# Performance work log

Hardware: AMD Instinct MI355X
Metric: run time of the kernel (lower is better)

Reference implementation:

```python
import jax, jax.numpy as jnp
import numpy as np

IMC = 256
EPS = 1e-6
BN_EPS = 1e-5
GRID = (69.12, 79.36)      # (depth, width) in meters
OFF = (0.0, -39.68, 0.0)   # (xoff, yoff, zoff)
RES = 0.64
ZMIN, ZMAX = -3.0, 2.76
SCALES = [0.25, 0.125, 0.0625, 0.03125, 0.015625]


def make_corners():
    # replicates make_grid(): corner lattice in lidar coords, shape [nz, nx, ny, 3]
    nx = int(round(GRID[0] / RES)) + 1   # 109
    ny = int(round(GRID[1] / RES)) + 1   # 125
    nz = int(round((ZMAX - ZMIN) / RES)) + 1  # 10
    xc = RES * np.arange(nx) + OFF[0]
    yc = GRID[1] - RES * np.arange(ny) + OFF[1]
    zc = ZMAX - RES * np.arange(nz)
    xx, yy = np.meshgrid(xc, yc, indexing='ij')
    base = np.stack([xx, yy, np.full_like(xx, OFF[2])], axis=-1)  # [nx,ny,3]
    zoffs = np.stack([np.zeros(nz), np.zeros(nz), zc], axis=-1)   # [nz,3]
    corners = base[None] + zoffs[:, None, None, :]
    return jnp.asarray(corners, jnp.float32)


def grid_sample(img, grid):
    # img [B,C,H,W]; grid [B,P,N,2] xy in [-1,1]; bilinear, zero padding, align_corners=False
    B, C, H, W = img.shape
    x = (grid[..., 0] + 1.0) * (W * 0.5) - 0.5
    y = (grid[..., 1] + 1.0) * (H * 0.5) - 0.5
    x0f = jnp.floor(x); y0f = jnp.floor(y)
    wx = (x - x0f).reshape(B, 1, -1)
    wy = (y - y0f).reshape(B, 1, -1)
    x0 = x0f.astype(jnp.int32); y0 = y0f.astype(jnp.int32)
    flat = img.reshape(B, C, H * W)
    def g(xi, yi):
        ok = ((xi >= 0) & (xi < W) & (yi >= 0) & (yi < H)).reshape(B, 1, -1)
        idx = (jnp.clip(yi, 0, H - 1) * W + jnp.clip(xi, 0, W - 1)).reshape(B, 1, -1)
        return jnp.take_along_axis(flat, idx, axis=2) * ok
    v00 = g(x0, y0); v01 = g(x0 + 1, y0); v10 = g(x0, y0 + 1); v11 = g(x0 + 1, y0 + 1)
    out = (v00 * (1 - wx) + v01 * wx) * (1 - wy) + (v10 * (1 - wx) + v11 * wx) * wy
    return out.reshape(B, C, grid.shape[1], grid.shape[2])


def oft(feats, calib, corners, scale, w, b):
    B, C, Hf, Wf = feats.shape
    # perspective projection of grid corners into the image plane
    hom = jnp.einsum('bij,zdwj->bzdwi', calib[:, :, :3], corners) + calib[:, None, None, None, :, 3]
    xy = hom[..., :2] / hom[..., 2:3]                      # [B,nz,nx,ny,2]
    img_size = jnp.array([Wf, Hf], jnp.float32) / scale
    nc = jnp.clip(2.0 * xy / img_size - 1.0, -1.0, 1.0)
    mn = jnp.minimum(nc[:, :-1, :-1, :-1], nc[:, :-1, 1:, :-1])
    mx = jnp.maximum(nc[:, 1:, 1:, 1:], nc[:, 1:, :-1, 1:])
    bbox = jnp.concatenate([mn, mx], axis=-1)              # [B,Zc,Dc,Wc,4]
    _, Zc, Dc, Wc, _ = bbox.shape
    bbox = bbox.reshape(B, Zc, Dc * Wc, 4)
    area = ((bbox[..., 2] - bbox[..., 0]) * (bbox[..., 3] - bbox[..., 1])
            * (Hf * Wf * 0.25) + EPS)[:, None]             # [B,1,Zc,N]
    visible = (area > EPS).astype(feats.dtype)
    ii = jnp.cumsum(jnp.cumsum(feats, axis=-1), axis=-2)   # integral image
    tl = grid_sample(ii, jnp.stack([bbox[..., 0], bbox[..., 1]], -1))
    br = grid_sample(ii, jnp.stack([bbox[..., 2], bbox[..., 3]], -1))
    tr = grid_sample(ii, jnp.stack([bbox[..., 2], bbox[..., 1]], -1))
    bl = grid_sample(ii, jnp.stack([bbox[..., 0], bbox[..., 3]], -1))
    vox = (tl + br - tr - bl) / area * visible             # [B,C,Zc,N]
    vox = vox.transpose(0, 3, 1, 2).reshape(B * Dc * Wc, C * Zc)
    ortho = jax.nn.relu(vox @ w.T + b).reshape(B, Dc, Wc, -1)
    return ortho.transpose(0, 3, 2, 1)                     # [B,imc,Wc,Dc]


def attention(x, aw, ab):
    s = jax.nn.sigmoid(x.mean(axis=(2, 3)) @ aw.T + ab)
    return x * s[:, :, None, None]


def conv3x3(x, w, stride):
    return jax.lax.conv_general_dilated(x, w, (stride, stride), ((1, 1), (1, 1)),
                                        dimension_numbers=('NCHW', 'OIHW', 'NCHW'))


def bn(x, g, b, m, v):
    scale = g / jnp.sqrt(v + BN_EPS)
    return (x - m[None, :, None, None]) * scale[None, :, None, None] + b[None, :, None, None]


def make_calib(B):
    K = np.array([[560.0, 0.0, 640.0], [0.0, 560.0, 192.0], [0.0, 0.0, 1.0]])
    Rt = np.array([[0.0, -1.0, 0.0, 0.05],   # lidar(x fwd, y left, z up) -> cam(x right, y down, z fwd)
                   [0.0, 0.0, -1.0, -0.30],
                   [1.0, 0.0, 0.0, 0.27]])
    P = K @ Rt
    return jnp.asarray(np.tile(P[None], (B, 1, 1)), jnp.float32)


def setup_inputs() -> dict:
    key = jax.random.key(0)
    ks = jax.random.split(key, 16)
    B = 1
    shapes = [(B, IMC, 96, 320), (B, IMC, 48, 160), (B, IMC, 24, 80), (B, IMC, 12, 40), (B, IMC, 6, 20)]
    feats = [jax.random.normal(ks[i], s, jnp.float32) * 0.1 for i, s in enumerate(shapes)]
    HC = 9 * IMC  # height_channels = int((2.76-(-3))/0.64 * 256) = 2304
    inp = {
        'feats04': feats[0], 'feats08': feats[1], 'feats16': feats[2],
        'feats32': feats[3], 'feats64': feats[4],
        'calib': make_calib(B),
        'oft_w': jax.random.normal(ks[5], (5, IMC, HC), jnp.float32) * 0.02,
        'oft_b': jax.random.normal(ks[6], (5, IMC), jnp.float32) * 0.02,
        'att_w': jax.random.normal(ks[7], (IMC, IMC), jnp.float32) * 0.05,
        'att_b': jnp.zeros((IMC,), jnp.float32),
        'conv1_w': jax.random.normal(ks[8], (IMC, IMC * 5, 3, 3), jnp.float32) * 0.02,
        'bn1_g': 1.0 + 0.1 * jax.random.normal(ks[9], (IMC,), jnp.float32),
        'bn1_b': 0.05 * jax.random.normal(ks[10], (IMC,), jnp.float32),
        'bn1_m': 0.05 * jax.random.normal(ks[11], (IMC,), jnp.float32),
        'bn1_v': jax.random.uniform(ks[12], (IMC,), jnp.float32, 0.5, 1.5),
        'conv2_w': jax.random.normal(ks[13], (IMC, IMC, 3, 3), jnp.float32) * 0.02,
        'bn2_g': 1.0 + 0.1 * jax.random.normal(ks[14], (IMC,), jnp.float32),
        'bn2_b': jnp.zeros((IMC,), jnp.float32),
        'bn2_m': jnp.zeros((IMC,), jnp.float32),
        'bn2_v': jax.random.uniform(ks[15], (IMC,), jnp.float32, 0.5, 1.5),
    }
    return inp


def reference(feats04, feats08, feats16, feats32, feats64, calib,
              oft_w, oft_b, att_w, att_b,
              conv1_w, bn1_g, bn1_b, bn1_m, bn1_v,
              conv2_w, bn2_g, bn2_b, bn2_m, bn2_v):
    corners = make_corners()
    feats = [feats04, feats08, feats16, feats32, feats64]
    orthos = [attention(oft(f, calib, corners, s, oft_w[i], oft_b[i]), att_w, att_b)
              for i, (f, s) in enumerate(zip(feats, SCALES))]
    x = jnp.concatenate(orthos, axis=1)            # [B, 5*imc, 124, 108]
    x = jax.nn.relu(bn(conv3x3(x, conv1_w, 2), bn1_g, bn1_b, bn1_m, bn1_v))
    x = jax.nn.relu(bn(conv3x3(x, conv2_w, 1), bn2_g, bn2_b, bn2_m, bn2_v))
    return x                                       # [B, imc, 62, 54]
```

## Files before the change

kernel.cpp:

```cpp
#include <hip/hip_runtime.h>

typedef __attribute__((ext_vector_type(8))) short short8;
typedef __attribute__((ext_vector_type(4))) float float4v;
typedef __attribute__((ext_vector_type(4))) int int4v;
typedef __attribute__((ext_vector_type(4))) unsigned short ushort4v;

#define NBOX 13392
#define ZC 9
#define KOFT 2304
#define NPIX 3348
#define NBLK0 105
#define NBLKC 27
#define TILEK 4096
#define NBSTRIDE 294912
#define VOXSZ 30965760

__device__ __forceinline__ unsigned short f2bf(float f) {
  union { float f; unsigned int i; } v; v.f = f;
  unsigned int r = v.i + 0x7FFFu + ((v.i >> 16) & 1u);
  return (unsigned short)(r >> 16);
}
__device__ __forceinline__ float bf2f(unsigned short u) {
  union { unsigned int i; float f; } v; v.i = ((unsigned int)u) << 16; return v.f;
}
__device__ __forceinline__ float i2f(int i) {
  union { int i; float f; } v; v.i = i; return v.f;
}

__device__ __forceinline__ const int* uniform_ptr(const int* p) {
  unsigned lo = (unsigned)(uintptr_t)p;
  unsigned hi = (unsigned)((uintptr_t)p >> 32);
  lo = (unsigned)__builtin_amdgcn_readfirstlane((int)lo);
  hi = (unsigned)__builtin_amdgcn_readfirstlane((int)hi);
  return (const int*)(((uintptr_t)hi << 32) | (uintptr_t)lo);
}

__device__ __forceinline__ void async16(const unsigned short* g, unsigned short* l) {
  __builtin_amdgcn_global_load_lds(
      (const __attribute__((address_space(1))) unsigned int*)g,
      (__attribute__((address_space(3))) unsigned int*)l, 16, 0, 0);
}

__global__ void k_alpha_beta(const float* __restrict__ oft_b,
                             const float* __restrict__ g1, const float* __restrict__ b1,
                             const float* __restrict__ m1, const float* __restrict__ v1,
                             const float* __restrict__ g2, const float* __restrict__ b2,
                             const float* __restrict__ m2, const float* __restrict__ v2,
                             float* __restrict__ ALPHA, float* __restrict__ BETA,
                             float* __restrict__ MEANS, unsigned short* __restrict__ ZPAGE) {
  int g = blockIdx.x, c = threadIdx.x;
  float al, be;
  if (g < 5) { al = 1.f; be = oft_b[g * 256 + c]; MEANS[g * 256 + c] = 0.f; }
  else {
    const float* gg = (g == 5) ? g1 : g2;
    const float* bb = (g == 5) ? b1 : b2;
    const float* mm = (g == 5) ? m1 : m2;
    const float* vv = (g == 5) ? v1 : v2;
    al = gg[c] / sqrtf(vv[c] + 1e-5f);
    be = bb[c] - mm[c] * al;
  }
  ALPHA[g * 256 + c] = al; BETA[g * 256 + c] = be;
  if (g == 0) ZPAGE[c] = 0;
}

__global__ void k_wpermT(const float* __restrict__ w, unsigned short* __restrict__ wp) {
  int idx = blockIdx.x * 256 + threadIdx.x;
  int sc = idx / 589824;
  int r  = idx % 589824;
  int j   = r & 7;
  int row = (r >> 3) & 127;
  int kc  = (r >> 10) & 3;
  int cs  = r >> 12;
  int cb  = cs / 72, s = cs % 72;
  int oc = cb * 128 + row;
  int k  = s * 32 + kc * 8 + j;
  int z = k >> 8, c = k & 255;
  wp[idx] = f2bf(w[((size_t)sc * 256 + oc) * 2304 + c * 9 + z]);
}

__global__ void k_wperm1T(const float* __restrict__ w, const float* __restrict__ satt,
                          unsigned short* __restrict__ wp) {
  int idx = blockIdx.x * 256 + threadIdx.x;
  int j   = idx & 7;
  int row = (idx >> 3) & 127;
  int kc  = (idx >> 10) & 3;
  int rest = idx >> 12;
  int s = rest % 40; rest /= 40;
  int r = rest % 9;  int cb = rest / 9;
  int oc = cb * 128 + row;
  int ic = s * 32 + kc * 8 + j;
  wp[idx] = f2bf(w[(size_t)oc * 11520 + ic * 9 + r] * satt[ic]);
}

__global__ void k_wperm2T(const float* __restrict__ w, unsigned short* __restrict__ wp) {
  int idx = blockIdx.x * 256 + threadIdx.x;
  int j   = idx & 7;
  int row = (idx >> 3) & 127;
  int kc  = (idx >> 10) & 3;
  int rest = idx >> 12;
  int s = rest % 8; rest /= 8;
  int r = rest % 9; int cb = rest / 9;
  int oc = cb * 128 + row;
  int ic = s * 32 + kc * 8 + j;
  wp[idx] = f2bf(w[(size_t)oc * 2304 + ic * 9 + r]);
}

__global__ void k_taps(const float* __restrict__ calib, int* __restrict__ taps,
                       int Hf, int Wf, float areaScale) {
  int idx = blockIdx.x * 256 + threadIdx.x;
  if (idx >= ZC * NBOX) return;
  int z = idx / NBOX, n = idx % NBOX;
  int d = n / 124, wj = n % 124;
  float P[12];
#pragma unroll
  for (int i = 0; i < 12; ++i) P[i] = calib[i];
  auto proj = [&](int k, int i, int j, float& nxo, float& nyo) {
    float X = 0.64f * (float)i;
    float Y = 39.68f - 0.64f * (float)j;
    float Z = 2.76f - 0.64f * (float)k;
    float hx = P[0] * X + P[1] * Y + P[2]  * Z + P[3];
    float hy = P[4] * X + P[5] * Y + P[6]  * Z + P[7];
    float hz = P[8] * X + P[9] * Y + P[10] * Z + P[11];
    float px = hx / hz, py = hy / hz;
    nxo = 2.f * px / 1280.f - 1.f; nxo = fminf(fmaxf(nxo, -1.f), 1.f);
    nyo = 2.f * py / 384.f  - 1.f; nyo = fminf(fmaxf(nyo, -1.f), 1.f);
  };
  float ax, ay, bx, by, cx, cy, dx, dy;
  proj(z,     d,     wj,     ax, ay);
  proj(z,     d + 1, wj,     bx, by);
  proj(z + 1, d + 1, wj + 1, cx, cy);
  proj(z + 1, d,     wj + 1, dx, dy);
  float x0 = fminf(ax, bx), y0 = fminf(ay, by);
  float x1 = fmaxf(cx, dx), y1 = fmaxf(cy, dy);
  float rawA = (x1 - x0) * (y1 - y0) * areaScale;
  int* ob = taps + (size_t)idx * 32;
  if (!(rawA > 0.f)) { ob[0] = 0; return; }
  float inv = 1.f / (rawA + 1e-6f);

  float u0 = (x0 + 1.f) * ((float)Wf * 0.5f) - 0.5f;
  float u1 = (x1 + 1.f) * ((float)Wf * 0.5f) - 0.5f;
  float fu0 = floorf(u0), fu1 = floorf(u1);
  int cx0 = (int)fu0, cx1 = (int)fu1;
  float wx0 = u0 - fu0, wx1 = u1 - fu1;
  int xs[4]; float xw[4];
  xs[0] = cx0; xs[1] = cx0 + 1; xs[2] = cx1; xs[3] = cx1 + 1;
  xw[0] = (1.f - wx0) * inv; xw[1] = wx0 * inv;
  xw[2] = -(1.f - wx1) * inv; xw[3] = -wx1 * inv;
  int dcx = cx1 - cx0;
  if (dcx == 0)      { xw[0] += xw[2]; xw[1] += xw[3]; xw[2] = 0.f; xw[3] = 0.f; }
  else if (dcx == 1) { xw[1] += xw[2]; xw[2] = xw[3]; xs[2] = xs[3]; xw[3] = 0.f; }
#pragma unroll
  for (int j = 0; j < 4; ++j) {
    if (xs[j] < 0 || xs[j] >= Wf) xw[j] = 0.f;
    xs[j] = min(max(xs[j], 0), Wf - 1);
  }
#define CSWX(a, b) { if (xw[a] == 0.f && xw[b] != 0.f) { \
    float tw = xw[a]; xw[a] = xw[b]; xw[b] = tw; \
    int ts = xs[a]; xs[a] = xs[b]; xs[b] = ts; } }
  CSWX(0, 1) CSWX(2, 3) CSWX(0, 2) CSWX(1, 3) CSWX(1, 2)
#undef CSWX
  int nx = (xw[0] != 0.f) + (xw[1] != 0.f) + (xw[2] != 0.f) + (xw[3] != 0.f);

  float v0 = (y0 + 1.f) * ((float)Hf * 0.5f) - 0.5f;
  float v1 = (y1 + 1.f) * ((float)Hf * 0.5f) - 0.5f;
  float fv0 = floorf(v0), fv1 = floorf(v1);
  int ry0 = (int)fv0, ry1 = (int)fv1;
  float wy0 = v0 - fv0, wy1 = v1 - fv1;
  int ys[4]; float yw[4];
  ys[0] = ry0; ys[1] = ry0 + 1; ys[2] = ry1; ys[3] = ry1 + 1;
  yw[0] = 1.f - wy0; yw[1] = wy0; yw[2] = -(1.f - wy1); yw[3] = -wy1;
  int dcy = ry1 - ry0;
  if (dcy == 0)      { yw[0] += yw[2]; yw[1] += yw[3]; yw[2] = 0.f; yw[3] = 0.f; }
  else if (dcy == 1) { yw[1] += yw[2]; yw[2] = yw[3]; ys[2] = ys[3]; yw[3] = 0.f; }
#pragma unroll
  for (int j = 0; j < 4; ++j) {
    if (ys[j] < 0 || ys[j] >= Hf) yw[j] = 0.f;
    ys[j] = min(max(ys[j], 0), Hf - 1);
  }
#define CSWY(a, b) { if (yw[a] == 0.f && yw[b] != 0.f) { \
    float tw = yw[a]; yw[a] = yw[b]; yw[b] = tw; \
    int ts = ys[a]; ys[a] = ys[b]; ys[b] = ts; } }
  CSWY(0, 1) CSWY(2, 3) CSWY(0, 2) CSWY(1, 3) CSWY(1, 2)
#undef CSWY
  int ny = (yw[0] != 0.f) + (yw[1] != 0.f) + (yw[2] != 0.f) + (yw[3] != 0.f);

  if (nx == 0 || ny == 0) { ob[0] = 0; return; }

  int off[16]; float w[16];
#pragma unroll
  for (int r = 0; r < 4; ++r)
#pragma unroll
    for (int c = 0; c < 4; ++c) {
      off[r * 4 + c] = (ys[r] * Wf + xs[c]) * 1024;
      w[r * 4 + c] = yw[r] * xw[c];
    }
  off[0] |= (nx << 25) | (ny << 28);
  int4v* obv = (int4v*)ob;
#pragma unroll
  for (int i = 0; i < 4; ++i)
    obv[i] = (int4v){off[4 * i], off[4 * i + 1], off[4 * i + 2], off[4 * i + 3]};
  float4v* wb = (float4v*)obv;
#pragma unroll
  for (int i = 0; i < 4; ++i)
    wb[4 + i] = (float4v){w[4 * i], w[4 * i + 1], w[4 * i + 2], w[4 * i + 3]};
}

__global__ void k_transpose_all(const float* __restrict__ f0, const float* __restrict__ f1,
                                const float* __restrict__ f2, const float* __restrict__ f3,
                                const float* __restrict__ f4, float* __restrict__ II) {
  int b = blockIdx.x;
  int sc, cx;
  if (b < 480)      { sc = 0; cx = b; }
  else if (b < 600) { sc = 1; cx = b - 480; }
  else if (b < 630) { sc = 2; cx = b - 600; }
  else if (b < 638) { sc = 3; cx = b - 630; }
  else              { sc = 4; cx = b - 638; }
  const int Ss[5] = {30720, 7680, 1920, 480, 120};
  const size_t IIof[5] = {0, 7864320, 9830400, 10321920, 10444800};
  const float* srcs[5] = {f0, f1, f2, f3, f4};
  int S = Ss[sc];
  const float* src = srcs[sc];
  float* dst = II + IIof[sc];
  __shared__ float tile[64][65];
  int t = threadIdx.x;
  int wave = t >> 6, lane = t & 63;
  int s0 = cx * 64, c0 = blockIdx.y * 64;
#pragma unroll
  for (int i = 0; i < 16; ++i) {
    int c_l = wave * 16 + i;
    if (s0 + lane < S) tile[c_l][lane] = src[(size_t)(c0 + c_l) * S + s0 + lane];
  }
  __syncthreads();
#pragma unroll
  for (int i = 0; i < 16; ++i) {
    int s_l = wave * 16 + i;
    if (s0 + s_l < S) dst[(size_t)(s0 + s_l) * 256 + c0 + lane] = tile[lane][s_l];
  }
}

__global__ void k_cumw_all(float* __restrict__ II) {
  int b = blockIdx.x;
  int sc, h;
  if (b < 96)       { sc = 0; h = b; }
  else if (b < 144) { sc = 1; h = b - 96; }
  else if (b < 168) { sc = 2; h = b - 144; }
  else if (b < 180) { sc = 3; h = b - 168; }
  else              { sc = 4; h = b - 180; }
  const int Wfs[5] = {320, 160, 80, 40, 20};
  const size_t IIof[5] = {0, 7864320, 9830400, 10321920, 10444800};
  int Wf = Wfs[sc];
  float* p = II + IIof[sc] + (size_t)h * Wf * 256 + threadIdx.x;
  float acc = 0.f;
#pragma unroll 4
  for (int w = 0; w < Wf; ++w) { acc += p[(size_t)w * 256]; p[(size_t)w * 256] = acc; }
}

__global__ void k_cumh_all(float* __restrict__ II) {
  int b = blockIdx.x;
  int sc, w;
  if (b < 320)      { sc = 0; w = b; }
  else if (b < 480) { sc = 1; w = b - 320; }
  else if (b < 560) { sc = 2; w = b - 480; }
  else if (b < 600) { sc = 3; w = b - 560; }
  else              { sc = 4; w = b - 600; }
  const int Wfs[5] = {320, 160, 80, 40, 20};
  const int Hfs[5] = {96, 48, 24, 12, 6};
  const size_t IIof[5] = {0, 7864320, 9830400, 10321920, 10444800};
  int Hf = Hfs[sc];
  size_t stride = (size_t)Wfs[sc] * 256;
  float* p = II + IIof[sc] + (size_t)w * 256 + threadIdx.x;
  float acc = 0.f;
#pragma unroll 4
  for (int h = 0; h < Hf; ++h) { acc += p[h * stride]; p[h * stride] = acc; }
}

__global__ __launch_bounds__(512) void k_sample(const float* __restrict__ ii,
                                                const int* __restrict__ taps,
                                                unsigned short* __restrict__ voxT) {
  __shared__ unsigned short st[3][8][66][4];
  int t = threadIdx.x;
  int wave = t >> 6, lane = t & 63;
  int n = blockIdx.x * 8 + wave;
  int zg = blockIdx.y * 3;
  const char* iib = (const char*)ii + (lane << 4);
#pragma unroll
  for (int dz = 0; dz < 3; ++dz) {
    int z = zg + dz;
    const int* tb = uniform_ptr(taps + (size_t)(z * NBOX + n) * 32);
    int o_[16];
#pragma unroll
    for (int i = 0; i < 16; ++i) o_[i] = tb[i];
    unsigned h = (unsigned)o_[0];
    int nx = (h >> 25) & 7;
    int ny = (h >> 28) & 7;
    o_[0] = (int)(h & 0x01FFFFFFu);
    ushort4v o;
    if (ny == 0) {
      o[0] = 0; o[1] = 0; o[2] = 0; o[3] = 0;
    } else {
      float w_[16];
#pragma unroll
      for (int i = 0; i < 16; ++i) w_[i] = i2f(tb[16 + i]);
      float4v a0 = {0.f, 0.f, 0.f, 0.f}, a1 = a0;
#define TAP(i, acc) { float4v t_ = *(const float4v*)(iib + (size_t)(unsigned)o_[i]); acc += t_ * w_[i]; }
      TAP(0, a0)
      if (nx > 1) TAP(1, a1)
      if (nx > 2) TAP(2, a0)
      if (nx > 3) TAP(3, a1)
      if (ny > 1) {
        TAP(4, a0)
        if (nx > 1) TAP(5, a1)
        if (nx > 2) TAP(6, a0)
        if (nx > 3) TAP(7, a1)
      }
      if (ny > 2) {
        TAP(8, a0)
        if (nx > 1) TAP(9, a1)
        if (nx > 2) TAP(10, a0)
        if (nx > 3) TAP(11, a1)
      }
      if (ny > 3) {
        TAP(12, a0)
        if (nx > 1) TAP(13, a1)
        if (nx > 2) TAP(14, a0)
        if (nx > 3) TAP(15, a1)
      }
#undef TAP
      float4v acc = a0 + a1;
#pragma unroll
      for (int j = 0; j < 4; ++j) o[j] = f2bf(acc[j]);
    }
    *(ushort4v*)&st[dz][wave][lane][0] = o;
  }
  __syncthreads();
  int nb = (blockIdx.x * 8) >> 7;
  int r0 = (blockIdx.x * 8) & 127;
  unsigned short* outb = voxT + (size_t)nb * NBSTRIDE + (size_t)r0 * 32;
  int lane32 = t & 31;
  int row = lane32 >> 2, kc = lane32 & 3;
#pragma unroll
  for (int p = 0; p < 2; ++p) {
    int q = p * 16 + (t >> 5);
    if (q < 24) {
      int zq = q >> 3;
      int si = q & 7;
      short8 v = *(const short8*)&st[zq][row][si * 8 + kc * 2][0];
      *(short8*)(outb + (size_t)(zg + zq) * 32768 + (size_t)si * 4096
                 + (size_t)(row * 32 + kc * 8)) = v;
    }
  }
}

__global__ __launch_bounds__(256) void k_gemmT_all(
    const unsigned short* __restrict__ AT, const unsigned short* __restrict__ BT,
    const float* __restrict__ beta, unsigned short* __restrict__ xbuf, int s0) {
  __shared__ unsigned short ls[8704];
  unsigned short* lsA = ls;
  unsigned short* lsB = ls + 4096;
  int t = threadIdx.x;
  int lane = t & 63, wave = t >> 6;
  int l15 = lane & 15, quad = lane >> 4;
  int nb = blockIdx.x, cb = blockIdx.y;
  int slab = blockIdx.z, sc = s0 + slab;
  int wrow = (wave >> 1) * 64, wcol = (wave & 1) * 64;

  const unsigned short* ga = AT + (size_t)slab * VOXSZ + (size_t)nb * NBSTRIDE + t * 8;
  const unsigned short* gb = BT + (size_t)sc * 589824 + (size_t)cb * NBSTRIDE + t * 8;
  unsigned short* ldA = lsA + t * 8;
  unsigned short* ldB = lsB + t * 8;

  float4v acc[4][4];
#pragma unroll
  for (int mi = 0; mi < 4; ++mi)
#pragma unroll
    for (int ni = 0; ni < 4; ++ni) acc[mi][ni] = (float4v){0.f, 0.f, 0.f, 0.f};

  for (int s = 0; s < 72; ++s) {
    async16(ga, ldA);
    async16(ga + 2048, ldA + 2048);
    async16(gb, ldB);
    async16(gb + 2048, ldB + 2048);
    ga += TILEK; gb += TILEK;
    __syncthreads();
    short8 af[4], bf[4];
    const short8* pA = (const short8*)lsA;
    const short8* pB = (const short8*)lsB;
#pragma unroll
    for (int mi = 0; mi < 4; ++mi) af[mi] = pA[(wrow + mi * 16 + l15) * 4 + quad];
#pragma unroll
    for (int ni = 0; ni < 4; ++ni) bf[ni] = pB[quad * 128 + wcol + ni * 16 + l15];
#pragma unroll
    for (int mi = 0; mi < 4; ++mi)
#pragma unroll
      for (int ni = 0; ni < 4; ++ni)
        acc[mi][ni] = __builtin_amdgcn_mfma_f32_16x16x32_bf16(af[mi], bf[ni], acc[mi][ni], 0, 0, 0);
    __syncthreads();
  }

  float bval[4];
#pragma unroll
  for (int ni = 0; ni < 4; ++ni)
    bval[ni] = beta[sc * 256 + cb * 128 + wcol + ni * 16 + l15];
#pragma unroll
  for (int ph = 0; ph < 2; ++ph) {
    if (wrow == ph * 64) {
#pragma unroll
      for (int mi = 0; mi < 4; ++mi)
#pragma unroll
        for (int ni = 0; ni < 4; ++ni)
#pragma unroll
          for (int j = 0; j < 4; ++j) {
            int row = mi * 16 + quad * 4 + j;
            int col = wcol + ni * 16 + l15;
            float v = acc[mi][ni][j] + bval[ni];
            ls[row * 136 + col] = f2bf(v > 0.f ? v : 0.f);
          }
    }
    __syncthreads();
#pragma unroll
    for (int it = 0; it < 4; ++it) {
      int idx = it * 256 + t;
      int row = idx >> 4, ch = idx & 15;
      int nn = nb * 128 + ph * 64 + row;
      if (nn < NBOX) {
        short8 v = *(const short8*)&ls[row * 136 + ch * 8];
        *(short8*)(xbuf + (size_t)nn * 1280 + sc * 256 + cb * 128 + ch * 8) = v;
      }
    }
    __syncthreads();
  }
}

__global__ __launch_bounds__(256) void k_gemmT(
    const unsigned short* __restrict__ AT, const unsigned short* __restrict__ BT,
    float* __restrict__ part) {
  __shared__ unsigned short lsA[4096];
  __shared__ unsigned short lsB[4096];
  int t = threadIdx.x;
  int lane = t & 63, wave = t >> 6;
  int l15 = lane & 15, quad = lane >> 4;
  int nb = blockIdx.x, cb = blockIdx.y, ks = blockIdx.z;
  int wrow = (wave >> 1) * 64, wcol = (wave & 1) * 64;

  const unsigned short* ga = AT + (size_t)nb * NBSTRIDE + (size_t)ks * 18 * TILEK + t * 8;
  const unsigned short* gb = BT + (size_t)cb * NBSTRIDE + (size_t)ks * 18 * TILEK + t * 8;
  unsigned short* ldA = lsA + t * 8;
  unsigned short* ldB = lsB + t * 8;

  float4v acc[4][4];
#pragma unroll
  for (int mi = 0; mi < 4; ++mi)
#pragma unroll
    for (int ni = 0; ni < 4; ++ni) acc[mi][ni] = (float4v){0.f, 0.f, 0.f, 0.f};

  for (int s = 0; s < 18; ++s) {
    async16(ga, ldA);
    async16(ga + 2048, ldA + 2048);
    async16(gb, ldB);
    async16(gb + 2048, ldB + 2048);
    ga += TILEK; gb += TILEK;
    __syncthreads();
    short8 af[4], bf[4];
    const short8* pA = (const short8*)lsA;
    const short8* pB = (const short8*)lsB;
#pragma unroll
    for (int mi = 0; mi < 4; ++mi) af[mi] = pA[(wrow + mi * 16 + l15) * 4 + quad];
#pragma unroll
    for (int ni = 0; ni < 4; ++ni) bf[ni] = pB[quad * 128 + wcol + ni * 16 + l15];
#pragma unroll
    for (int mi = 0; mi < 4; ++mi)
#pragma unroll
      for (int ni = 0; ni < 4; ++ni)
        acc[mi][ni] = __builtin_amdgcn_mfma_f32_16x16x32_bf16(af[mi], bf[ni], acc[mi][ni], 0, 0, 0);
    __syncthreads();
  }

#pragma unroll
  for (int mi = 0; mi < 4; ++mi) {
    int nb0 = nb * 128 + wrow + mi * 16 + quad * 4;
#pragma unroll
    for (int j = 0; j < 4; ++j) {
      int nn = nb0 + j;
      if (nn < NBOX) {
#pragma unroll
        for (int ni = 0; ni < 4; ++ni) {
          int oc = cb * 128 + wcol + ni * 16 + l15;
          part[((size_t)ks * NBOX + nn) * 256 + oc] = acc[mi][ni][j];
        }
      }
    }
  }
}

__global__ void k_redoft(const float* __restrict__ part, const float* __restrict__ beta,
                         unsigned short* __restrict__ xbuf, int choff) {
  int n = blockIdx.x, oc = threadIdx.x;
  float v = part[(size_t)n * 256 + oc]
          + part[((size_t)NBOX + n) * 256 + oc]
          + part[((size_t)2 * NBOX + n) * 256 + oc]
          + part[((size_t)3 * NBOX + n) * 256 + oc];
  v += beta[oc];
  v = v > 0.f ? v : 0.f;
  xbuf[(size_t)n * 1280 + choff + oc] = f2bf(v);
}

template <int MODE>
__global__ __launch_bounds__(256) void k_gemmS(
    const unsigned short* __restrict__ A, const unsigned short* __restrict__ BT,
    float* __restrict__ part, const unsigned short* __restrict__ zpage) {
  constexpr int KIC   = (MODE == 1) ? 1280 : 256;
  constexpr int STEPS = KIC / 32;
  __shared__ unsigned short lsA[4096];
  __shared__ unsigned short lsB[4096];
  int t = threadIdx.x;
  int lane = t & 63, wave = t >> 6;
  int l15 = lane & 15, quad = lane >> 4;
  int n0 = blockIdx.x * 128, oc0 = blockIdx.y * 128;
  int r = blockIdx.z;
  int wrow = (wave >> 1) * 64, wcol = (wave & 1) * 64;
  int srow = t & 127, skc = t >> 7;

  int p = n0 + srow;
  int oy = p / 54, ox = p - oy * 54;
  int ky = r / 3, kx = r - ky * 3;
  bool valid; int sp;
  if (MODE == 1) {
    int ih = 2 * oy + ky - 1, iw = 2 * ox + kx - 1;
    valid = (p < NPIX) && ((unsigned)ih < 124u) && ((unsigned)iw < 108u);
    sp = iw * 124 + ih;
  } else {
    int ih = oy + ky - 1, iw = ox + kx - 1;
    valid = (p < NPIX) && ((unsigned)ih < 62u) && ((unsigned)iw < 54u);
    sp = ih * 54 + iw;
  }
  const unsigned short* ga = valid ? (A + (size_t)sp * KIC + skc * 8) : zpage;
  int astep = valid ? 32 : 0;
  const unsigned short* gb = BT + ((size_t)(blockIdx.y * 9 + r) * STEPS) * TILEK + t * 8;
  unsigned short* ldA = lsA + t * 8;
  unsigned short* ldB = lsB + t * 8;

  float4v acc[4][4];
#pragma unroll
  for (int mi = 0; mi < 4; ++mi)
#pragma unroll
    for (int ni = 0; ni < 4; ++ni) acc[mi][ni] = (float4v){0.f, 0.f, 0.f, 0.f};

  for (int s = 0; s < STEPS; ++s) {
    async16(ga, ldA);
    async16(ga + 16, ldA + 2048);
    async16(gb, ldB);
    async16(gb + 2048, ldB + 2048);
    ga += astep; gb += TILEK;
    __syncthreads();
    short8 af[4], bf[4];
    const short8* pA = (const short8*)lsA;
    const short8* pB = (const short8*)lsB;
#pragma unroll
    for (int mi = 0; mi < 4; ++mi) af[mi] = pA[quad * 128 + wrow + mi * 16 + l15];
#pragma unroll
    for (int ni = 0; ni < 4; ++ni) bf[ni] = pB[quad * 128 + wcol + ni * 16 + l15];
#pragma unroll
    for (int mi = 0; mi < 4; ++mi)
#pragma unroll
      for (int ni = 0; ni < 4; ++ni)
        acc[mi][ni] = __builtin_amdgcn_mfma_f32_16x16x32_bf16(af[mi], bf[ni], acc[mi][ni], 0, 0, 0);
    __syncthreads();
  }

#pragma unroll
  for (int mi = 0; mi < 4; ++mi) {
    int nb0 = n0 + wrow + mi * 16 + quad * 4;
#pragma unroll
    for (int j = 0; j < 4; ++j) {
      int nn = nb0 + j;
      if (nn < NPIX) {
#pragma unroll
        for (int ni = 0; ni < 4; ++ni) {
          int oc = oc0 + wcol + ni * 16 + l15;
          part[((size_t)r * NPIX + nn) * 256 + oc] = acc[mi][ni][j];
        }
      }
    }
  }
}

template <bool F32OUT>
__global__ void k_redconv(const float* __restrict__ part, const float* __restrict__ alpha,
                          const float* __restrict__ beta, void* __restrict__ outv) {
  int p = blockIdx.x, oc = threadIdx.x;
  float v = 0.f;
#pragma unroll
  for (int r = 0; r < 9; ++r) v += part[((size_t)r * NPIX + p) * 256 + oc];
  v = v * alpha[oc] + beta[oc];
  v = v > 0.f ? v : 0.f;
  if (F32OUT) ((float*)outv)[(size_t)oc * NPIX + p] = v;
  else ((unsigned short*)outv)[(size_t)p * 256 + oc] = f2bf(v);
}

__global__ void k_means2(const unsigned short* __restrict__ x, float* __restrict__ means) {
  int tid = threadIdx.x;
  int r0 = blockIdx.x * 64;
  float part[5] = {0.f, 0.f, 0.f, 0.f, 0.f};
  for (int i = 0; i < 64; ++i) {
    int row = r0 + i;
    if (row < NBOX) {
      const unsigned short* rp = x + (size_t)row * 1280;
#pragma unroll
      for (int g = 0; g < 5; ++g) part[g] += bf2f(rp[g * 256 + tid]);
    }
  }
#pragma unroll
  for (int g = 0; g < 5; ++g) atomicAdd(&means[g * 256 + tid], part[g]);
}

__global__ void k_att(const float* __restrict__ means, const float* __restrict__ aw,
                      const float* __restrict__ ab, float* __restrict__ satt) {
  int sc = blockIdx.x, c = threadIdx.x;
  __shared__ float m[256];
  m[c] = means[sc * 256 + c] * (1.f / (float)NBOX);
  __syncthreads();
  float acc = ab[c];
  for (int j = 0; j < 256; ++j) acc += m[j] * aw[c * 256 + j];
  satt[sc * 256 + c] = 1.f / (1.f + expf(-acc));
}

extern "C" void kernel_launch(void* const* d_in, const int* in_sizes, int n_in,
                              void* d_out, int out_size, void* d_ws, size_t ws_size,
                              hipStream_t stream) {
  const float* feats[5];
  for (int i = 0; i < 5; ++i) feats[i] = (const float*)d_in[i];
  const float* calib   = (const float*)d_in[5];
  const float* oft_w   = (const float*)d_in[6];
  const float* oft_b   = (const float*)d_in[7];
  const float* att_w   = (const float*)d_in[8];
  const float* att_b   = (const float*)d_in[9];
  const float* conv1_w = (const float*)d_in[10];
  const float* bn1g = (const float*)d_in[11];
  const float* bn1b = (const float*)d_in[12];
  const float* bn1m = (const float*)d_in[13];
  const float* bn1v = (const float*)d_in[14];
  const float* conv2_w = (const float*)d_in[15];
  const float* bn2g = (const float*)d_in[16];
  const float* bn2b = (const float*)d_in[17];
  const float* bn2m = (const float*)d_in[18];
  const float* bn2v = (const float*)d_in[19];

  char* ws = (char*)d_ws;
  size_t off = 0;
  auto alloc = [&](size_t bytes) -> void* {
    void* p = ws + off; off += (bytes + 255) & ~(size_t)255; return p;
  };
  unsigned short* WPERMT = (unsigned short*)alloc((size_t)5 * 589824 * 2);
  unsigned short* WC1T   = (unsigned short*)alloc((size_t)2949120 * 2);
  unsigned short* WC2T   = (unsigned short*)alloc((size_t)589824 * 2);
  float*          II     = (float*)alloc((size_t)10475520 * 4);
  unsigned short* XBUF   = (unsigned short*)alloc((size_t)NBOX * 1280 * 2);
  unsigned short* Y1     = (unsigned short*)alloc((size_t)NPIX * 256 * 2);
  float*          MEANS  = (float*)alloc(1280 * 4);
  float*          SATT   = (float*)alloc(1280 * 4);
  float*          ALPHA  = (float*)alloc(7 * 256 * 4);
  float*          BETA   = (float*)alloc(7 * 256 * 4);
  unsigned short* ZPAGE  = (unsigned short*)alloc(256 * 2);

  const size_t SLAB   = (size_t)VOXSZ * 2;
  const size_t TAPSZ  = (size_t)ZC * NBOX * 128;
  const size_t PARTSZ = (size_t)4 * NBOX * 256 * 4;
  size_t rem = (ws_size > off) ? ws_size - off : 0;

  int NS;
  int* TAPS; unsigned short* VOXT; float* PART;
  if (rem >= 5 * SLAB) {
    NS = 5;
    VOXT = (unsigned short*)alloc(5 * SLAB);
    TAPS = (int*)XBUF;
    PART = (float*)VOXT;
  } else if (rem >= 2 * SLAB + TAPSZ) {
    NS = (int)((rem - TAPSZ) / SLAB); if (NS > 4) NS = 4;
    TAPS = (int*)alloc(TAPSZ);
    VOXT = (unsigned short*)alloc((size_t)NS * SLAB);
    PART = (float*)VOXT;
  } else {
    NS = 0;
    VOXT = (unsigned short*)alloc(SLAB);
    PART = (float*)alloc(PARTSZ);
    TAPS = (int*)PART;
  }
  (void)in_sizes; (void)n_in; (void)out_size;

  static const int HFs[5] = {96, 48, 24, 12, 6};
  static const int WFs[5] = {320, 160, 80, 40, 20};
  static const size_t IIoff[5] = {0, 7864320, 9830400, 10321920, 10444800};

  k_alpha_beta<<<7, 256, 0, stream>>>(oft_b, bn1g, bn1b, bn1m, bn1v,
                                      bn2g, bn2b, bn2m, bn2v, ALPHA, BETA, MEANS, ZPAGE);
  k_wpermT<<<11520, 256, 0, stream>>>(oft_w, WPERMT);
  k_wperm2T<<<2304, 256, 0, stream>>>(conv2_w, WC2T);

  k_transpose_all<<<dim3(640, 4), 256, 0, stream>>>(feats[0], feats[1], feats[2],
                                                    feats[3], feats[4], II);
  k_cumw_all<<<186, 256, 0, stream>>>(II);
  k_cumh_all<<<620, 256, 0, stream>>>(II);

  if (NS > 0) {
    int g0 = 0;
    while (g0 < 5) {
      int gsz = 5 - g0; if (gsz > NS) gsz = NS;
      for (int s = g0; s < g0 + gsz; ++s) {
        k_taps<<<(ZC * NBOX + 255) / 256, 256, 0, stream>>>(
            calib, TAPS, HFs[s], WFs[s], (float)(HFs[s] * WFs[s]) * 0.25f);
        k_sample<<<dim3(NBOX / 8, 3), 512, 0, stream>>>(
            II + IIoff[s], TAPS, VOXT + (size_t)(s - g0) * VOXSZ);
      }
      k_gemmT_all<<<dim3(NBLK0, 2, gsz), 256, 0, stream>>>(VOXT, WPERMT, BETA, XBUF, g0);
      g0 += gsz;
    }
  } else {
    for (int s = 0; s < 5; ++s) {
      k_taps<<<(ZC * NBOX + 255) / 256, 256, 0, stream>>>(
          calib, TAPS, HFs[s], WFs[s], (float)(HFs[s] * WFs[s]) * 0.25f);
      k_sample<<<dim3(NBOX / 8, 3), 512, 0, stream>>>(II + IIoff[s], TAPS, VOXT);
      k_gemmT<<<dim3(NBLK0, 2, 4), 256, 0, stream>>>(
          VOXT, WPERMT + (size_t)s * 589824, PART);
      k_redoft<<<NBOX, 256, 0, stream>>>(PART, BETA + s * 256, XBUF, s * 256);
    }
  }

  k_means2<<<(NBOX + 63) / 64, 256, 0, stream>>>(XBUF, MEANS);
  k_att<<<5, 256, 0, stream>>>(MEANS, att_w, att_b, SATT);
  k_wperm1T<<<11520, 256, 0, stream>>>(conv1_w, SATT, WC1T);

  k_gemmS<1><<<dim3(NBLKC, 2, 9), 256, 0, stream>>>(XBUF, WC1T, PART, ZPAGE);
  k_redconv<false><<<NPIX, 256, 0, stream>>>(PART, ALPHA + 5 * 256, BETA + 5 * 256, Y1);

  k_gemmS<2><<<dim3(NBLKC, 2, 9), 256, 0, stream>>>(Y1, WC2T, PART, ZPAGE);
  k_redconv<true><<<NPIX, 256, 0, stream>>>(PART, ALPHA + 6 * 256, BETA + 6 * 256, d_out);
}
```

Before: 847.6 us.

## Fuse tap computation into sampling kernel and vectorize means reduction

Replaces the separate k_taps pass, which wrote per-box tap offsets and weights to global memory, with k_sampleF. This kernel recomputes the corner projection and integral-image tap setup in registers before gathering. It removes one launch per scale and the tap buffer's global write and read traffic, at the cost of redundant per-lane projection arithmetic. k_means2 also now reads 8 bf16 values per thread with vector loads, and the tap workspace allocation is dropped so more slabs may fit in the middle allocation path.

```diff
diff --git a/kernel.cpp b/kernel.cpp
--- a/kernel.cpp
+++ b/kernel.cpp
@@ -274,6 +274,159 @@
   for (int h = 0; h < Hf; ++h) { acc += p[h * stride]; p[h * stride] = acc; }
 }
 
+__global__ __launch_bounds__(512) void k_sampleF(const float* __restrict__ ii,
+                                                 const float* __restrict__ calib,
+                                                 unsigned short* __restrict__ voxT,
+                                                 int Hf, int Wf, float areaScale) {
+  __shared__ unsigned short st[3][8][66][4];
+  int t = threadIdx.x;
+  int wave = t >> 6, lane = t & 63;
+  int n = blockIdx.x * 8 + wave;
+  int zg = blockIdx.y * 3;
+  int d = n / 124, wj = n % 124;
+  float P[12];
+#pragma unroll
+  for (int i = 0; i < 12; ++i) P[i] = calib[i];
+  const char* iib = (const char*)ii + (lane << 4);
+  auto proj = [&](int k, int i, int j, float& nxo, float& nyo) {
+    float X = 0.64f * (float)i;
+    float Y = 39.68f - 0.64f * (float)j;
+    float Z = 2.76f - 0.64f * (float)k;
+    float hx = P[0] * X + P[1] * Y + P[2]  * Z + P[3];
+    float hy = P[4] * X + P[5] * Y + P[6]  * Z + P[7];
+    float hz = P[8] * X + P[9] * Y + P[10] * Z + P[11];
+    float px = hx / hz, py = hy / hz;
+    nxo = 2.f * px / 1280.f - 1.f; nxo = fminf(fmaxf(nxo, -1.f), 1.f);
+    nyo = 2.f * py / 384.f  - 1.f; nyo = fminf(fmaxf(nyo, -1.f), 1.f);
+  };
+#pragma unroll
+  for (int dz = 0; dz < 3; ++dz) {
+    int z = zg + dz;
+    float ax, ay, bx, by, cx, cy, dx, dy;
+    proj(z,     d,     wj,     ax, ay);
+    proj(z,     d + 1, wj,     bx, by);
+    proj(z + 1, d + 1, wj + 1, cx, cy);
+    proj(z + 1, d,     wj + 1, dx, dy);
+    float x0 = fminf(ax, bx), y0 = fminf(ay, by);
+    float x1 = fmaxf(cx, dx), y1 = fmaxf(cy, dy);
+    float rawA = (x1 - x0) * (y1 - y0) * areaScale;
+    int nx = 0, ny = 0;
+    int o_[16]; float w_[16];
+    if (rawA > 0.f) {
+      float inv = 1.f / (rawA + 1e-6f);
+      float u0 = (x0 + 1.f) * ((float)Wf * 0.5f) - 0.5f;
+      float u1 = (x1 + 1.f) * ((float)Wf * 0.5f) - 0.5f;
+      float fu0 = floorf(u0), fu1 = floorf(u1);
+      int cx0 = (int)fu0, cx1 = (int)fu1;
+      float wx0 = u0 - fu0, wx1 = u1 - fu1;
+      int xs[4]; float xw[4];
+      xs[0] = cx0; xs[1] = cx0 + 1; xs[2] = cx1; xs[3] = cx1 + 1;
+      xw[0] = (1.f - wx0) * inv; xw[1] = wx0 * inv;
+      xw[2] = -(1.f - wx1) * inv; xw[3] = -wx1 * inv;
+      int dcx = cx1 - cx0;
+      if (dcx == 0)      { xw[0] += xw[2]; xw[1] += xw[3]; xw[2] = 0.f; xw[3] = 0.f; }
+      else if (dcx == 1) { xw[1] += xw[2]; xw[2] = xw[3]; xs[2] = xs[3]; xw[3] = 0.f; }
+#pragma unroll
+      for (int j = 0; j < 4; ++j) {
+        if (xs[j] < 0 || xs[j] >= Wf) xw[j] = 0.f;
+        xs[j] = min(max(xs[j], 0), Wf - 1);
+      }
+#define CSWX(a, b) { if (xw[a] == 0.f && xw[b] != 0.f) { \
+    float tw = xw[a]; xw[a] = xw[b]; xw[b] = tw; \
+    int ts = xs[a]; xs[a] = xs[b]; xs[b] = ts; } }
+      CSWX(0, 1) CSWX(2, 3) CSWX(0, 2) CSWX(1, 3) CSWX(1, 2)
+#undef CSWX
+      nx = (xw[0] != 0.f) + (xw[1] != 0.f) + (xw[2] != 0.f) + (xw[3] != 0.f);
+
+      float v0 = (y0 + 1.f) * ((float)Hf * 0.5f) - 0.5f;
+      float v1 = (y1 + 1.f) * ((float)Hf * 0.5f) - 0.5f;
+      float fv0 = floorf(v0), fv1 = floorf(v1);
+      int ry0 = (int)fv0, ry1 = (int)fv1;
+      float wy0 = v0 - fv0, wy1 = v1 - fv1;
+      int ys[4]; float yw[4];
+      ys[0] = ry0; ys[1] = ry0 + 1; ys[2] = ry1; ys[3] = ry1 + 1;
+      yw[0] = 1.f - wy0; yw[1] = wy0; yw[2] = -(1.f - wy1); yw[3] = -wy1;
+      int dcy = ry1 - ry0;
+      if (dcy == 0)      { yw[0] += yw[2]; yw[1] += yw[3]; yw[2] = 0.f; yw[3] = 0.f; }
+      else if (dcy == 1) { yw[1] += yw[2]; yw[2] = yw[3]; ys[2] = ys[3]; yw[3] = 0.f; }
+#pragma unroll
+      for (int j = 0; j < 4; ++j) {
+        if (ys[j] < 0 || ys[j] >= Hf) yw[j] = 0.f;
+        ys[j] = min(max(ys[j], 0), Hf - 1);
+      }
+#define CSWY(a, b) { if (yw[a] == 0.f && yw[b] != 0.f) { \
+    float tw = yw[a]; yw[a] = yw[b]; yw[b] = tw; \
+    int ts = ys[a]; ys[a] = ys[b]; ys[b] = ts; } }
+      CSWY(0, 1) CSWY(2, 3) CSWY(0, 2) CSWY(1, 3) CSWY(1, 2)
+#undef CSWY
+      ny = (yw[0] != 0.f) + (yw[1] != 0.f) + (yw[2] != 0.f) + (yw[3] != 0.f);
+      if (nx == 0) ny = 0;
+      if (ny != 0) {
+#pragma unroll
+        for (int r = 0; r < 4; ++r)
+#pragma unroll
+          for (int c = 0; c < 4; ++c) {
+            o_[r * 4 + c] = (ys[r] * Wf + xs[c]) * 1024;
+            w_[r * 4 + c] = yw[r] * xw[c];
+          }
+      }
+    }
+    nx = __builtin_amdgcn_readfirstlane(nx);
+    ny = __builtin_amdgcn_readfirstlane(ny);
+    ushort4v o;
+    if (ny == 0) {
+      o[0] = 0; o[1] = 0; o[2] = 0; o[3] = 0;
+    } else {
+      float4v a0 = {0.f, 0.f, 0.f, 0.f}, a1 = a0;
+#define TAP(i, acc) { float4v t_ = *(const float4v*)(iib + (size_t)(unsigned)o_[i]); acc += t_ * w_[i]; }
+      TAP(0, a0)
+      if (nx > 1) TAP(1, a1)
+      if (nx > 2) TAP(2, a0)
+      if (nx > 3) TAP(3, a1)
+      if (ny > 1) {
+        TAP(4, a0)
+        if (nx > 1) TAP(5, a1)
+        if (nx > 2) TAP(6, a0)
+        if (nx > 3) TAP(7, a1)
+      }
+      if (ny > 2) {
+        TAP(8, a0)
+        if (nx > 1) TAP(9, a1)
+        if (nx > 2) TAP(10, a0)
+        if (nx > 3) TAP(11, a1)
+      }
+      if (ny > 3) {
+        TAP(12, a0)
+        if (nx > 1) TAP(13, a1)
+        if (nx > 2) TAP(14, a0)
+        if (nx > 3) TAP(15, a1)
+      }
+#undef TAP
+      float4v acc = a0 + a1;
+#pragma unroll
+      for (int j = 0; j < 4; ++j) o[j] = f2bf(acc[j]);
+    }
+    *(ushort4v*)&st[dz][wave][lane][0] = o;
+  }
+  __syncthreads();
+  int nb = (blockIdx.x * 8) >> 7;
+  int r0 = (blockIdx.x * 8) & 127;
+  unsigned short* outb = voxT + (size_t)nb * NBSTRIDE + (size_t)r0 * 32;
+  int lane32 = t & 31;
+  int row = lane32 >> 2, kc = lane32 & 3;
+#pragma unroll
+  for (int p = 0; p < 2; ++p) {
+    int q = p * 16 + (t >> 5);
+    if (q < 24) {
+      int zq = q >> 3;
+      int si = q & 7;
+      short8 v = *(const short8*)&st[zq][row][si * 8 + kc * 2][0];
+      *(short8*)(outb + (size_t)(zg + zq) * 32768 + (size_t)si * 4096
+                 + (size_t)(row * 32 + kc * 8)) = v;
+    }
+  }
+}
+
 __global__ __launch_bounds__(512) void k_sample(const float* __restrict__ ii,
                                                 const int* __restrict__ taps,
                                                 unsigned short* __restrict__ voxT) {
@@ -599,18 +752,20 @@
 
 __global__ void k_means2(const unsigned short* __restrict__ x, float* __restrict__ means) {
   int tid = threadIdx.x;
+  if (tid >= 160) return;
+  int c0 = tid * 8;
   int r0 = blockIdx.x * 64;
-  float part[5] = {0.f, 0.f, 0.f, 0.f, 0.f};
+  float part[8] = {0.f, 0.f, 0.f, 0.f, 0.f, 0.f, 0.f, 0.f};
   for (int i = 0; i < 64; ++i) {
     int row = r0 + i;
     if (row < NBOX) {
-      const unsigned short* rp = x + (size_t)row * 1280;
-#pragma unroll
-      for (int g = 0; g < 5; ++g) part[g] += bf2f(rp[g * 256 + tid]);
-    }
-  }
-#pragma unroll
-  for (int g = 0; g < 5; ++g) atomicAdd(&means[g * 256 + tid], part[g]);
+      short8 v = *(const short8*)(x + (size_t)row * 1280 + c0);
+#pragma unroll
+      for (int j = 0; j < 8; ++j) part[j] += bf2f((unsigned short)v[j]);
+    }
+  }
+#pragma unroll
+  for (int j = 0; j < 8; ++j) atomicAdd(&means[c0 + j], part[j]);
 }
 
 __global__ void k_att(const float* __restrict__ means, const float* __restrict__ aw,
@@ -663,20 +818,17 @@
   unsigned short* ZPAGE  = (unsigned short*)alloc(256 * 2);
 
   const size_t SLAB   = (size_t)VOXSZ * 2;
-  const size_t TAPSZ  = (size_t)ZC * NBOX * 128;
   const size_t PARTSZ = (size_t)4 * NBOX * 256 * 4;
   size_t rem = (ws_size > off) ? ws_size - off : 0;
 
   int NS;
-  int* TAPS; unsigned short* VOXT; float* PART;
+  int* TAPS = nullptr; unsigned short* VOXT; float* PART;
   if (rem >= 5 * SLAB) {
     NS = 5;
     VOXT = (unsigned short*)alloc(5 * SLAB);
-    TAPS = (int*)XBUF;
     PART = (float*)VOXT;
-  } else if (rem >= 2 * SLAB + TAPSZ) {
-    NS = (int)((rem - TAPSZ) / SLAB); if (NS > 4) NS = 4;
-    TAPS = (int*)alloc(TAPSZ);
+  } else if (rem >= 2 * SLAB) {
+    NS = (int)(rem / SLAB); if (NS > 4) NS = 4;
     VOXT = (unsigned short*)alloc((size_t)NS * SLAB);
     PART = (float*)VOXT;
   } else {
@@ -706,10 +858,9 @@
     while (g0 < 5) {
       int gsz = 5 - g0; if (gsz > NS) gsz = NS;
       for (int s = g0; s < g0 + gsz; ++s) {
-        k_taps<<<(ZC * NBOX + 255) / 256, 256, 0, stream>>>(
-            calib, TAPS, HFs[s], WFs[s], (float)(HFs[s] * WFs[s]) * 0.25f);
-        k_sample<<<dim3(NBOX / 8, 3), 512, 0, stream>>>(
-            II + IIoff[s], TAPS, VOXT + (size_t)(s - g0) * VOXSZ);
+        k_sampleF<<<dim3(NBOX / 8, 3), 512, 0, stream>>>(
+            II + IIoff[s], calib, VOXT + (size_t)(s - g0) * VOXSZ,
+            HFs[s], WFs[s], (float)(HFs[s] * WFs[s]) * 0.25f);
       }
       k_gemmT_all<<<dim3(NBLK0, 2, gsz), 256, 0, stream>>>(VOXT, WPERMT, BETA, XBUF, g0);
       g0 += gsz;
```

Result: slower. 1.074 ms (+26.7%).
